# Kernel tuning notes

Measured on AMD Instinct MI355X. Metric: run time of the kernel, lower is better.

The kernel has to match this reference:

```python
import jax, jax.numpy as jnp
import numpy as np

SCALE_BASE = 512.0
GN_EPS = 1e-5


def _xpos(x, downscale):
    # x: [..., L, D]; XPOS rotary embedding with exponential length scale (torchscale)
    L, D = x.shape[-2], x.shape[-1]
    half = D // 2
    base = (jnp.arange(0, D, 2, dtype=jnp.float32) + 0.4 * D) / (1.4 * D)  # [half]
    min_pos = -(L // 2)
    power = (jnp.arange(min_pos, min_pos + L, dtype=jnp.float32) / SCALE_BASE)[:, None]
    scale = base[None, :] ** power  # [L, half]
    inv_freq = 1.0 / (10000.0 ** (jnp.arange(half, dtype=jnp.float32) / half))
    ang = jnp.arange(L, dtype=jnp.float32)[:, None] * inv_freq[None, :]  # [L, half]
    sin, cos = jnp.sin(ang), jnp.cos(ang)
    if downscale:
        scale = 1.0 / scale
    sin_s = jnp.repeat(sin * scale, 2, axis=-1)  # duplicate_interleave -> [L, D]
    cos_s = jnp.repeat(cos * scale, 2, axis=-1)
    x1, x2 = x[..., ::2], x[..., 1::2]
    rot = jnp.stack((-x2, x1), axis=-1).reshape(x.shape)  # rotate_every_two
    return x * cos_s + rot * sin_s


def _decay_mask(L, H):
    gammas = 1.0 - jnp.exp(jnp.linspace(np.log(1.0 / 32.0), np.log(1.0 / 512.0), H)).astype(jnp.float32)
    idx = jnp.arange(L)
    dist = idx[:, None] - idx[None, :]  # [L, L]
    causal = dist >= 0
    d = jnp.maximum(dist, 0).astype(jnp.float32)
    # gamma^|n-s| below diagonal, 0 above (gamma^inf = 0 in the torch version)
    return jnp.where(causal[None], gammas[:, None, None] ** d[None], 0.0)  # [H, L, L]


def setup_inputs() -> dict:
    key = jax.random.key(0)
    ks = jax.random.split(key, 9)
    B, L, D, H = 2, 2048, 1024, 16
    hd = D // H
    return {
        "query": jax.random.normal(ks[0], (B, L, D), jnp.float32),
        "key": jax.random.normal(ks[1], (B, L, D), jnp.float32),
        "value": jax.random.normal(ks[2], (B, L, D), jnp.float32),
        "W_Q": jax.random.normal(ks[3], (H, D, hd), jnp.float32) / D,
        "W_K": jax.random.normal(ks[4], (H, D, hd), jnp.float32) / D,
        "W_V": jax.random.normal(ks[5], (H, D, hd), jnp.float32) / D,
        "g_w": jax.random.normal(ks[6], (D, D), jnp.float32) * (2.0 / (D + D)) ** 0.5,
        "g_b": jnp.zeros((D,), jnp.float32),
        "out_w": jax.random.normal(ks[7], (D, D), jnp.float32) * (2.0 / (D + D)) ** 0.5,
        "out_b": jnp.zeros((D,), jnp.float32),
    }


def reference(query, key, value, W_Q, W_K, W_V, g_w, g_b, out_w, out_b):
    B, L, D = query.shape
    H = W_Q.shape[0]
    q = jnp.einsum('bld,hde->bhle', query, W_Q)
    k = jnp.einsum('bld,hde->bhle', key, W_K)
    v = jnp.einsum('bld,hde->bhle', value, W_V)
    q = _xpos(q, downscale=False)
    k = _xpos(k, downscale=True)
    # retention_parallel: QK^T * decay mask (no softmax, no scale), then @ V
    sim = jnp.einsum('bhnd,bhsd->bhns', q, k) * _decay_mask(L, H)[None]
    ret = jnp.einsum('bhns,bhsd->bhnd', sim, v)  # [B, H, L, hd]
    # GroupNorm(num_groups=H, affine=False) on (b n, h d): normalize per (b, h, n) over hd
    mu = ret.mean(axis=-1, keepdims=True)
    var = ret.var(axis=-1, keepdims=True)
    ret = (ret - mu) / jnp.sqrt(var + GN_EPS)
    ret = ret.transpose(0, 2, 1, 3).reshape(B, L, D)  # b h n d -> b n (h d)
    gate = jax.nn.silu(query @ g_w.T + g_b)
    return (ret * gate) @ out_w.T + out_b
```

## Files before the change

### kernel.cpp

```cpp
#include <hip/hip_runtime.h>
#include <cstdint>

#define B_  2
#define L_  2048
#define D_  1024
#define H_  16
#define HD_ 64
#define M_  (B_*L_)

#define MD  4194304u
#define DD  1048576u

#define OFF_XQB  0u
#define OFF_XKB  (MD)
#define OFF_XVB  (2u*MD)
#define OFF_WQT  (3u*MD)
#define OFF_WKT  (3u*MD + DD)
#define OFF_WVT  (3u*MD + 2u*DD)
#define OFF_GWB  (3u*MD + 3u*DD)
#define OFF_OWB  (3u*MD + 4u*DD)
#define OFF_GATE (3u*MD + 5u*DD)
#define OFF_QB2  (OFF_GATE + MD)
#define OFF_KB2  (OFF_QB2 + MD)
#define OFF_VTG  (OFF_KB2 + MD)
#define OFF_ABUF (OFF_VTG + MD)
#define OFF_F32  (OFF_ABUF + MD)

typedef __attribute__((ext_vector_type(8))) short bf16x8;
typedef __attribute__((ext_vector_type(4))) float f32x4;

__device__ __forceinline__ unsigned short f2b(float x){
  union { float f; unsigned u; } a; a.f = x;
  unsigned r = a.u + 0x7FFFu + ((a.u >> 16) & 1u);
  return (unsigned short)(r >> 16);
}
__device__ __forceinline__ float b2f(unsigned short u){
  union { unsigned u; float f; } a; a.u = ((unsigned)u) << 16; return a.f;
}

__global__ __launch_bounds__(256) void prep_kernel(
    const float* __restrict__ q, const float* __restrict__ k,
    const float* __restrict__ v, const float* __restrict__ gw,
    const float* __restrict__ ow, const float* __restrict__ WQ,
    const float* __restrict__ WK, const float* __restrict__ WV,
    unsigned short* __restrict__ ws)
{
  __shared__ float t[32][33];
  const int bx = blockIdx.x, tid = threadIdx.x;
  if (bx < 14336) {
    size_t i = ((size_t)bx * 256 + tid) * 4;
    const float* src; unsigned short* dst;
    if (i < MD)            { src = q  + i;              dst = ws + OFF_XQB + i; }
    else if (i < 2u*MD)    { src = k  + (i - MD);       dst = ws + OFF_XKB + (i - MD); }
    else if (i < 3u*MD)    { src = v  + (i - 2u*MD);    dst = ws + OFF_XVB + (i - 2u*MD); }
    else if (i < 3u*MD+DD) { src = gw + (i - 3u*MD);    dst = ws + OFF_GWB + (i - 3u*MD); }
    else                   { src = ow + (i - 3u*MD-DD); dst = ws + OFF_OWB + (i - 3u*MD - DD); }
    float4 vv = *(const float4*)src;
    ushort4 o; o.x = f2b(vv.x); o.y = f2b(vv.y); o.z = f2b(vv.z); o.w = f2b(vv.w);
    *(ushort4*)dst = o;
  } else if (bx < 17408) {
    const int tb = bx - 14336;
    const int w = tb >> 10;
    const int tb2 = tb & 1023;
    const int h = tb2 >> 6, tt = tb2 & 63;
    const int e0 = (tt & 1) * 32, d0 = (tt >> 1) * 32;
    const float* in = (w == 0) ? WQ : (w == 1) ? WK : WV;
    unsigned short* out = ws + ((w == 0) ? OFF_WQT : (w == 1) ? OFF_WKT : OFF_WVT);
    const int x = tid & 31, y0 = tid >> 5;
    for (int yy = y0; yy < 32; yy += 8)
      t[yy][x] = in[((size_t)h * D_ + d0 + yy) * HD_ + e0 + x];
    __syncthreads();
    for (int yy = y0; yy < 32; yy += 8)
      out[((size_t)h * HD_ + e0 + yy) * D_ + d0 + x] = f2b(t[x][yy]);
  } else {
    float* fb = (float*)(ws + OFF_F32);
    const int idx = (bx - 17408) * 256 + tid;
    const int l = idx >> 5, i = idx & 31;
    const float base = (2.0f * (float)i + 0.4f * (float)HD_) / (1.4f * (float)HD_);
    const float p = (float)(l - L_ / 2) * (1.0f / 512.0f);
    const float sc = exp2f(p * log2f(base));
    const float invf = exp2f(-(float)i * (13.287712379549449f / 32.0f));
    float s, c; sincosf((float)l * invf, &s, &c);
    fb[          l * 32 + i] = c * sc;
    fb[ 65536 +  l * 32 + i] = s * sc;
    const float is = 1.0f / sc;
    fb[131072 +  l * 32 + i] = c * is;
    fb[196608 +  l * 32 + i] = s * is;
  }
}

__device__ __forceinline__ void gemm_body(
    const unsigned short* __restrict__ A, const unsigned short* __restrict__ Bt,
    float* __restrict__ outF, unsigned short* __restrict__ outB,
    const float* __restrict__ ct, const float* __restrict__ st,
    const float* __restrict__ bias, int mode, int ldc, int M0, int N0,
    char* As, char* Bs)
{
  const int tid = threadIdx.x;
  const int wave = tid >> 6, lane = tid & 63;
  const int wm = wave & 1, wn = wave >> 1;
  const int mlane = lane & 15, kgrp = lane >> 4;
  const int srow = lane >> 2;
  const int scs  = lane & 3;
  const char* Ab = (const char*)A;
  const char* Bb = (const char*)Bt;

  f32x4 acc[4][4] = {};

  for (int K0 = 0; K0 < 1024; K0 += 32) {
    __syncthreads();
#pragma unroll
    for (int t = 0; t < 2; ++t) {
      const int row = wave * 32 + t * 16 + srow;
      const int gc = scs ^ ((row >> 1) & 3);
      const char* ga = Ab + ((size_t)(M0 + row) * 1024 + K0 + gc * 8) * 2;
      __builtin_amdgcn_global_load_lds(
          (const __attribute__((address_space(1))) void*)ga,
          (__attribute__((address_space(3))) void*)(As + (wave * 32 + t * 16) * 64 + lane * 16),
          16, 0, 0);
      const char* gb = Bb + ((size_t)(N0 + row) * 1024 + K0 + gc * 8) * 2;
      __builtin_amdgcn_global_load_lds(
          (const __attribute__((address_space(1))) void*)gb,
          (__attribute__((address_space(3))) void*)(Bs + (wave * 32 + t * 16) * 64 + lane * 16),
          16, 0, 0);
    }
    __syncthreads();
    bf16x8 af[4], bfr[4];
#pragma unroll
    for (int tm = 0; tm < 4; ++tm) {
      const int r = wm * 64 + tm * 16 + mlane;
      af[tm] = *(const bf16x8*)(As + r * 64 + ((kgrp ^ ((r >> 1) & 3)) << 4));
    }
#pragma unroll
    for (int tn = 0; tn < 4; ++tn) {
      const int r = wn * 64 + tn * 16 + mlane;
      bfr[tn] = *(const bf16x8*)(Bs + r * 64 + ((kgrp ^ ((r >> 1) & 3)) << 4));
    }
#pragma unroll
    for (int tm = 0; tm < 4; ++tm)
#pragma unroll
      for (int tn = 0; tn < 4; ++tn)
        acc[tm][tn] = __builtin_amdgcn_mfma_f32_16x16x32_bf16(af[tm], bfr[tn], acc[tm][tn], 0, 0, 0);
  }

#pragma unroll
  for (int tm = 0; tm < 4; ++tm)
#pragma unroll
    for (int tn = 0; tn < 4; ++tn) {
      f32x4 v = acc[tm][tn];
#pragma unroll
      for (int r = 0; r < 4; ++r) {
        const int grow = M0 + wm * 64 + tm * 16 + (lane >> 4) * 4 + r;
        const int gcol = N0 + wn * 64 + tn * 16 + mlane;
        float val = v[r];
        if (mode == 1 || mode == 2) {
          const float partner = __shfl_xor(val, 1);
          const int l = grow & (L_ - 1);
          const int i = (gcol >> 1) & 31;
          const float c = ct[l * 32 + i], s = st[l * 32 + i];
          val = (gcol & 1) ? (val * c + partner * s) : (val * c - partner * s);
          outB[(size_t)grow * ldc + gcol] = f2b(val);
        } else if (mode == 0) {
          outB[(size_t)grow * ldc + gcol] = f2b(val);
        } else if (mode == 3) {
          const float x = val + bias[gcol];
          outB[(size_t)grow * ldc + gcol] = f2b(x / (1.0f + expf(-x)));
        } else {
          outF[(size_t)grow * ldc + gcol] = val + bias[gcol];
        }
      }
    }
}

__global__ __launch_bounds__(256) void gemm4_kernel(
    unsigned short* __restrict__ ws, const float* __restrict__ g_b)
{
  __shared__ __align__(16) char As[128 * 64];
  __shared__ __align__(16) char Bs[128 * 64];
  const int z = blockIdx.y, bx = blockIdx.x;
  float* fb = (float*)(ws + OFF_F32);
  if (z == 0 && bx == 0 && threadIdx.x == 0)
    ((unsigned*)(fb + 262144))[0] = 0;
  const unsigned short *A, *Bt; unsigned short* outB;
  const float *ct = nullptr, *st = nullptr, *bias = nullptr;
  int mode, ldc, M0, N0;
  if (z == 0) {
    A = ws + OFF_XQB; Bt = ws + OFF_WQT; outB = ws + OFF_QB2;
    ct = fb; st = fb + 65536; mode = 1; ldc = D_;
    M0 = (bx & 31) * 128; N0 = (bx >> 5) * 128;
  } else if (z == 1) {
    A = ws + OFF_XKB; Bt = ws + OFF_WKT; outB = ws + OFF_KB2;
    ct = fb + 131072; st = fb + 196608; mode = 2; ldc = D_;
    M0 = (bx & 31) * 128; N0 = (bx >> 5) * 128;
  } else if (z == 2) {
    A = ws + OFF_WVT; Bt = ws + OFF_XVB; outB = ws + OFF_VTG;
    mode = 0; ldc = M_;
    M0 = (bx & 7) * 128; N0 = (bx >> 3) * 128;
  } else {
    A = ws + OFF_XQB; Bt = ws + OFF_GWB; outB = ws + OFF_GATE;
    bias = g_b; mode = 3; ldc = D_;
    M0 = (bx & 31) * 128; N0 = (bx >> 5) * 128;
  }
  gemm_body(A, Bt, nullptr, outB, ct, st, bias, mode, ldc, M0, N0, As, Bs);
}

__global__ __launch_bounds__(256) void gemm_final_kernel(
    unsigned short* __restrict__ ws, const float* __restrict__ out_b,
    float* __restrict__ out)
{
  __shared__ __align__(16) char As[128 * 64];
  __shared__ __align__(16) char Bs[128 * 64];
  gemm_body(ws + OFF_ABUF, ws + OFF_OWB, out, nullptr, nullptr, nullptr,
            out_b, 4, D_, blockIdx.x * 128, blockIdx.y * 128, As, Bs);
}

#define AQ_OFF 0
#define AK_OFF 8192
#define AV_OFF 16384
#define AP_OFF 24576

__global__ __launch_bounds__(256) void attn_mfma_kernel(
    const unsigned short* __restrict__ qg, const unsigned short* __restrict__ kg,
    const unsigned short* __restrict__ vtg, const unsigned short* __restrict__ gate,
    unsigned short* __restrict__ Abuf, unsigned* __restrict__ ctr)
{
  __shared__ __align__(16) char smem[32768];
  __shared__ unsigned s_item;
  const int tid = threadIdx.x, wave = tid >> 6, lane = tid & 63;
  const int mlane = lane & 15, kgrp = lane >> 4;
  const int rl = lane >> 3, csel = lane & 7;

  const float lo   = -3.4657359027997265f;
  const float step = -0.1848392481493187f;

  for (;;) {
    __syncthreads();
    if (tid == 0) s_item = atomicAdd(ctr, 1u);
    __syncthreads();
    const unsigned j = s_item;
    if (j >= 1024u) break;
    const int xq = 31 - (int)(j >> 5);
    const int bh = (int)(j & 31u), b = bh >> 4, h = bh & 15;
    const int l0 = xq * 64;

    const float gamma = 1.0f - expf(lo + (float)h * step);
    const float lg2g  = log2f(gamma);
    const float g1    = exp2f(-lg2g);
    const float gmr[4] = {1.0f, g1, g1 * g1, g1 * g1 * g1};

#pragma unroll
    for (int t = 0; t < 2; ++t) {
      const int row = 16 * wave + 8 * t + rl;
      const char* g = (const char*)(qg + (size_t)(b * L_ + l0 + row) * D_ + h * HD_ + ((csel ^ (row & 7)) << 3));
      __builtin_amdgcn_global_load_lds(
          (const __attribute__((address_space(1))) void*)g,
          (__attribute__((address_space(3))) void*)(smem + AQ_OFF + (16 * wave + 8 * t) * 128 + lane * 16),
          16, 0, 0);
    }
    __syncthreads();

    bf16x8 qa[2];
    {
      const int row = 16 * wave + mlane;
#pragma unroll
      for (int kk = 0; kk < 2; ++kk)
        qa[kk] = *(const bf16x8*)(smem + AQ_OFF + row * 128 + (((4 * kk + kgrp) ^ (row & 7)) << 4));
    }
    const float rqm = exp2f((float)(l0 + 16 * wave + mlane) * lg2g);

    f32x4 racc[4] = {};

    for (int it = 0; it <= xq; ++it) {
      const int s0 = it * 64;
      __syncthreads();
#pragma unroll
      for (int t = 0; t < 2; ++t) {
        const int row = 16 * wave + 8 * t + rl;
        const char* gk = (const char*)(kg + (size_t)(b * L_ + s0 + row) * D_ + h * HD_ + ((csel ^ (row & 7)) << 3));
        __builtin_amdgcn_global_load_lds(
            (const __attribute__((address_space(1))) void*)gk,
            (__attribute__((address_space(3))) void*)(smem + AK_OFF + (16 * wave + 8 * t) * 128 + lane * 16),
            16, 0, 0);
        const char* gv = (const char*)(vtg + (size_t)(h * HD_ + row) * M_ + b * L_ + s0 + ((csel ^ (row & 7)) << 3));
        __builtin_amdgcn_global_load_lds(
            (const __attribute__((address_space(1))) void*)gv,
            (__attribute__((address_space(3))) void*)(smem + AV_OFF + (16 * wave + 8 * t) * 128 + lane * 16),
            16, 0, 0);
      }
      __syncthreads();

      bf16x8 kb[4][2], vb[4][2];
#pragma unroll
      for (int tn = 0; tn < 4; ++tn)
#pragma unroll
        for (int kk = 0; kk < 2; ++kk) {
          const int row = 16 * tn + mlane;
          const int sw = ((4 * kk + kgrp) ^ (row & 7)) << 4;
          kb[tn][kk] = *(const bf16x8*)(smem + AK_OFF + row * 128 + sw);
          vb[tn][kk] = *(const bf16x8*)(smem + AV_OFF + row * 128 + sw);
        }
      float csb[4];
#pragma unroll
      for (int tn = 0; tn < 4; ++tn)
        csb[tn] = exp2f(-(float)(s0 + 16 * tn + 4 * kgrp) * lg2g);

      f32x4 sf[4];
#pragma unroll
      for (int tn = 0; tn < 4; ++tn) {
        f32x4 z = {};
        z = __builtin_amdgcn_mfma_f32_16x16x32_bf16(kb[tn][0], qa[0], z, 0, 0, 0);
        sf[tn] = __builtin_amdgcn_mfma_f32_16x16x32_bf16(kb[tn][1], qa[1], z, 0, 0, 0);
      }
      const int nrow = l0 + 16 * wave + mlane;
      const bool needMask = (it == xq);
      const int prow = 16 * wave + mlane;
#pragma unroll
      for (int tn = 0; tn < 4; ++tn) {
        const float wbase = rqm * csb[tn];
        const int sbase = s0 + 16 * tn + 4 * kgrp;
        float vv[4];
#pragma unroll
        for (int r = 0; r < 4; ++r) {
          float w = wbase * gmr[r];
          if (needMask) w = (nrow - (sbase + r) >= 0) ? w : 0.0f;
          vv[r] = sf[tn][r] * w;
        }
        uint2 pk;
        pk.x = (unsigned)f2b(vv[0]) | ((unsigned)f2b(vv[1]) << 16);
        pk.y = (unsigned)f2b(vv[2]) | ((unsigned)f2b(vv[3]) << 16);
        *(uint2*)(smem + AP_OFF + prow * 128 +
                  (((2 * tn + (kgrp >> 1)) ^ (prow & 7)) << 4) + ((kgrp & 1) << 3)) = pk;
      }
      bf16x8 pa[2];
#pragma unroll
      for (int kk = 0; kk < 2; ++kk) {
        const int row = 16 * wave + mlane;
        pa[kk] = *(const bf16x8*)(smem + AP_OFF + row * 128 + (((4 * kk + kgrp) ^ (row & 7)) << 4));
      }
#pragma unroll
      for (int tn = 0; tn < 4; ++tn) {
        racc[tn] = __builtin_amdgcn_mfma_f32_16x16x32_bf16(pa[0], vb[tn][0], racc[tn], 0, 0, 0);
        racc[tn] = __builtin_amdgcn_mfma_f32_16x16x32_bf16(pa[1], vb[tn][1], racc[tn], 0, 0, 0);
      }
    }

#pragma unroll
    for (int r = 0; r < 4; ++r) {
      float vv[4], sm = 0.0f, sq = 0.0f;
#pragma unroll
      for (int tn = 0; tn < 4; ++tn) {
        vv[tn] = racc[tn][r];
        sm += vv[tn]; sq += vv[tn] * vv[tn];
      }
#pragma unroll
      for (int off = 1; off < 16; off <<= 1) {
        sm += __shfl_xor(sm, off);
        sq += __shfl_xor(sq, off);
      }
      const float mu = sm * (1.0f / 64.0f);
      float var = sq * (1.0f / 64.0f) - mu * mu;
      var = fmaxf(var, 0.0f);
      const float inv = rsqrtf(var + 1e-5f);
      const int row = l0 + 16 * wave + kgrp * 4 + r;
      const size_t base = (size_t)(b * L_ + row) * D_ + h * HD_;
#pragma unroll
      for (int tn = 0; tn < 4; ++tn) {
        const int c = 16 * tn + mlane;
        const float g = b2f(gate[base + c]);
        Abuf[base + c] = f2b((vv[tn] - mu) * inv * g);
      }
    }
  }
}

extern "C" void kernel_launch(void* const* d_in, const int* in_sizes, int n_in,
                              void* d_out, int out_size, void* d_ws, size_t ws_size,
                              hipStream_t stream)
{
  const float* query = (const float*)d_in[0];
  const float* key   = (const float*)d_in[1];
  const float* value = (const float*)d_in[2];
  const float* W_Q   = (const float*)d_in[3];
  const float* W_K   = (const float*)d_in[4];
  const float* W_V   = (const float*)d_in[5];
  const float* g_b   = (const float*)d_in[7];
  const float* out_b = (const float*)d_in[9];
  float* out = (float*)d_out;

  unsigned short* ws = (unsigned short*)d_ws;
  float* fb = (float*)(ws + OFF_F32);
  unsigned* ctr = (unsigned*)(fb + 262144);

  prep_kernel<<<17664, 256, 0, stream>>>(query, key, value,
                                         (const float*)d_in[6],
                                         (const float*)d_in[8],
                                         W_Q, W_K, W_V, ws);

  gemm4_kernel<<<dim3(256, 4), 256, 0, stream>>>(ws, g_b);

  attn_mfma_kernel<<<512, 256, 0, stream>>>(ws + OFF_QB2, ws + OFF_KB2,
                                            ws + OFF_VTG, ws + OFF_GATE,
                                            ws + OFF_ABUF, ctr);

  gemm_final_kernel<<<dim3(32, 8), 256, 0, stream>>>(ws, out_b, out);
}
```

Before: 268.7 us.

## Retile GEMMs to 128x64 with K=64 steps and statically pair attention work

The shared GEMM body moves from 128x128 tiles with 32-wide K steps to 128x64 tiles with 64-wide K steps and an 8-way XOR swizzle. The GEMM grids double, so there are more blocks to fill the compute units, and there are half as many K-loop barriers. The attention kernel drops its atomic work-queue counter. Each block now handles a fixed pair of query tiles (p and 31-p) to balance the causal workload, and a __syncthreads is added before P is read back from LDS. In exchange, each block reuses less A data and issues an extra barrier per attention iteration.

```diff
diff --git a/kernel.cpp b/kernel.cpp
--- a/kernel.cpp
+++ b/kernel.cpp
@@ -27,6 +27,7 @@
 #define OFF_F32  (OFF_ABUF + MD)
 
 typedef __attribute__((ext_vector_type(8))) short bf16x8;
+typedef __attribute__((ext_vector_type(4))) short s16x4;
 typedef __attribute__((ext_vector_type(4))) float f32x4;
 
 __device__ __forceinline__ unsigned short f2b(float x){
@@ -100,58 +101,65 @@
   const int wave = tid >> 6, lane = tid & 63;
   const int wm = wave & 1, wn = wave >> 1;
   const int mlane = lane & 15, kgrp = lane >> 4;
-  const int srow = lane >> 2;
-  const int scs  = lane & 3;
+  const int rl = lane >> 3, csel = lane & 7;
   const char* Ab = (const char*)A;
   const char* Bb = (const char*)Bt;
 
-  f32x4 acc[4][4] = {};
-
-  for (int K0 = 0; K0 < 1024; K0 += 32) {
+  f32x4 acc[4][2] = {};
+
+  for (int K0 = 0; K0 < 1024; K0 += 64) {
     __syncthreads();
 #pragma unroll
-    for (int t = 0; t < 2; ++t) {
-      const int row = wave * 32 + t * 16 + srow;
-      const int gc = scs ^ ((row >> 1) & 3);
-      const char* ga = Ab + ((size_t)(M0 + row) * 1024 + K0 + gc * 8) * 2;
+    for (int t = 0; t < 4; ++t) {
+      const int row = wave * 32 + t * 8 + rl;
+      const int gc = csel ^ (row & 7);
+      const char* ga = Ab + ((size_t)(M0 + row) * 1024 + K0) * 2 + gc * 16;
       __builtin_amdgcn_global_load_lds(
           (const __attribute__((address_space(1))) void*)ga,
-          (__attribute__((address_space(3))) void*)(As + (wave * 32 + t * 16) * 64 + lane * 16),
+          (__attribute__((address_space(3))) void*)(As + (wave * 32 + t * 8) * 128 + lane * 16),
           16, 0, 0);
-      const char* gb = Bb + ((size_t)(N0 + row) * 1024 + K0 + gc * 8) * 2;
+    }
+#pragma unroll
+    for (int t = 0; t < 2; ++t) {
+      const int row = wave * 16 + t * 8 + rl;
+      const int gc = csel ^ (row & 7);
+      const char* gb = Bb + ((size_t)(N0 + row) * 1024 + K0) * 2 + gc * 16;
       __builtin_amdgcn_global_load_lds(
           (const __attribute__((address_space(1))) void*)gb,
-          (__attribute__((address_space(3))) void*)(Bs + (wave * 32 + t * 16) * 64 + lane * 16),
+          (__attribute__((address_space(3))) void*)(Bs + (wave * 16 + t * 8) * 128 + lane * 16),
           16, 0, 0);
     }
     __syncthreads();
-    bf16x8 af[4], bfr[4];
-#pragma unroll
-    for (int tm = 0; tm < 4; ++tm) {
-      const int r = wm * 64 + tm * 16 + mlane;
-      af[tm] = *(const bf16x8*)(As + r * 64 + ((kgrp ^ ((r >> 1) & 3)) << 4));
-    }
-#pragma unroll
-    for (int tn = 0; tn < 4; ++tn) {
-      const int r = wn * 64 + tn * 16 + mlane;
-      bfr[tn] = *(const bf16x8*)(Bs + r * 64 + ((kgrp ^ ((r >> 1) & 3)) << 4));
-    }
-#pragma unroll
-    for (int tm = 0; tm < 4; ++tm)
-#pragma unroll
-      for (int tn = 0; tn < 4; ++tn)
-        acc[tm][tn] = __builtin_amdgcn_mfma_f32_16x16x32_bf16(af[tm], bfr[tn], acc[tm][tn], 0, 0, 0);
+#pragma unroll
+    for (int kh = 0; kh < 2; ++kh) {
+      bf16x8 af[4], bfr[2];
+#pragma unroll
+      for (int tm = 0; tm < 4; ++tm) {
+        const int r = wm * 64 + tm * 16 + mlane;
+        af[tm] = *(const bf16x8*)(As + r * 128 + (((kh * 4 + kgrp) ^ (r & 7)) << 4));
+      }
+#pragma unroll
+      for (int tn = 0; tn < 2; ++tn) {
+        const int r = wn * 32 + tn * 16 + mlane;
+        bfr[tn] = *(const bf16x8*)(Bs + r * 128 + (((kh * 4 + kgrp) ^ (r & 7)) << 4));
+      }
+#pragma unroll
+      for (int tm = 0; tm < 4; ++tm)
+#pragma unroll
+        for (int tn = 0; tn < 2; ++tn)
+          acc[tm][tn] = __builtin_amdgcn_mfma_f32_16x16x32_bf16(af[tm], bfr[tn], acc[tm][tn], 0, 0, 0);
+    }
   }
 
 #pragma unroll
   for (int tm = 0; tm < 4; ++tm)
 #pragma unroll
-    for (int tn = 0; tn < 4; ++tn) {
+    for (int tn = 0; tn < 2; ++tn) {
       f32x4 v = acc[tm][tn];
 #pragma unroll
       for (int r = 0; r < 4; ++r) {
         const int grow = M0 + wm * 64 + tm * 16 + (lane >> 4) * 4 + r;
-        const int gcol = N0 + wn * 64 + tn * 16 + mlane;
+        const int gcol = N0 + wn * 32 + tn * 16 + mlane;
         float val = v[r];
         if (mode == 1 || mode == 2) {
           const float partner = __shfl_xor(val, 1);
@@ -175,31 +183,29 @@
 __global__ __launch_bounds__(256) void gemm4_kernel(
     unsigned short* __restrict__ ws, const float* __restrict__ g_b)
 {
-  __shared__ __align__(16) char As[128 * 64];
-  __shared__ __align__(16) char Bs[128 * 64];
+  __shared__ __align__(16) char As[128 * 128];
+  __shared__ __align__(16) char Bs[64 * 128];
   const int z = blockIdx.y, bx = blockIdx.x;
   float* fb = (float*)(ws + OFF_F32);
-  if (z == 0 && bx == 0 && threadIdx.x == 0)
-    ((unsigned*)(fb + 262144))[0] = 0;
   const unsigned short *A, *Bt; unsigned short* outB;
   const float *ct = nullptr, *st = nullptr, *bias = nullptr;
   int mode, ldc, M0, N0;
   if (z == 0) {
     A = ws + OFF_XQB; Bt = ws + OFF_WQT; outB = ws + OFF_QB2;
     ct = fb; st = fb + 65536; mode = 1; ldc = D_;
-    M0 = (bx & 31) * 128; N0 = (bx >> 5) * 128;
+    M0 = (bx & 31) * 128; N0 = (bx >> 5) * 64;
   } else if (z == 1) {
     A = ws + OFF_XKB; Bt = ws + OFF_WKT; outB = ws + OFF_KB2;
     ct = fb + 131072; st = fb + 196608; mode = 2; ldc = D_;
-    M0 = (bx & 31) * 128; N0 = (bx >> 5) * 128;
+    M0 = (bx & 31) * 128; N0 = (bx >> 5) * 64;
   } else if (z == 2) {
     A = ws + OFF_WVT; Bt = ws + OFF_XVB; outB = ws + OFF_VTG;
     mode = 0; ldc = M_;
-    M0 = (bx & 7) * 128; N0 = (bx >> 3) * 128;
+    M0 = (bx & 7) * 128; N0 = (bx >> 3) * 64;
   } else {
     A = ws + OFF_XQB; Bt = ws + OFF_GWB; outB = ws + OFF_GATE;
     bias = g_b; mode = 3; ldc = D_;
-    M0 = (bx & 31) * 128; N0 = (bx >> 5) * 128;
+    M0 = (bx & 31) * 128; N0 = (bx >> 5) * 64;
   }
   gemm_body(A, Bt, nullptr, outB, ct, st, bias, mode, ldc, M0, N0, As, Bs);
 }
@@ -208,10 +214,10 @@
     unsigned short* __restrict__ ws, const float* __restrict__ out_b,
     float* __restrict__ out)
 {
-  __shared__ __align__(16) char As[128 * 64];
-  __shared__ __align__(16) char Bs[128 * 64];
+  __shared__ __align__(16) char As[128 * 128];
+  __shared__ __align__(16) char Bs[64 * 128];
   gemm_body(ws + OFF_ABUF, ws + OFF_OWB, out, nullptr, nullptr, nullptr,
-            out_b, 4, D_, blockIdx.x * 128, blockIdx.y * 128, As, Bs);
+            out_b, 4, D_, blockIdx.x * 128, blockIdx.y * 64, As, Bs);
 }
 
 #define AQ_OFF 0
@@ -222,32 +228,30 @@
 __global__ __launch_bounds__(256) void attn_mfma_kernel(
     const unsigned short* __restrict__ qg, const unsigned short* __restrict__ kg,
     const unsigned short* __restrict__ vtg, const unsigned short* __restrict__ gate,
-    unsigned short* __restrict__ Abuf, unsigned* __restrict__ ctr)
+    unsigned short* __restrict__ Abuf)
 {
   __shared__ __align__(16) char smem[32768];
-  __shared__ unsigned s_item;
   const int tid = threadIdx.x, wave = tid >> 6, lane = tid & 63;
   const int mlane = lane & 15, kgrp = lane >> 4;
   const int rl = lane >> 3, csel = lane & 7;
 
+  const int id = blockIdx.x;
+  const int bh = id & 31, p = id >> 5;
+  const int b = bh >> 4, h = bh & 15;
+
   const float lo   = -3.4657359027997265f;
   const float step = -0.1848392481493187f;
-
-  for (;;) {
+  const float gamma = 1.0f - expf(lo + (float)h * step);
+  const float lg2g  = log2f(gamma);
+  const float g1    = exp2f(-lg2g);
+  const float gmr[4] = {1.0f, g1, g1 * g1, g1 * g1 * g1};
+
+#pragma unroll 1
+  for (int half = 0; half < 2; ++half) {
+    const int xq = half ? (31 - p) : p;
+    const int l0 = xq * 64;
+
     __syncthreads();
-    if (tid == 0) s_item = atomicAdd(ctr, 1u);
-    __syncthreads();
-    const unsigned j = s_item;
-    if (j >= 1024u) break;
-    const int xq = 31 - (int)(j >> 5);
-    const int bh = (int)(j & 31u), b = bh >> 4, h = bh & 15;
-    const int l0 = xq * 64;
-
-    const float gamma = 1.0f - expf(lo + (float)h * step);
-    const float lg2g  = log2f(gamma);
-    const float g1    = exp2f(-lg2g);
-    const float gmr[4] = {1.0f, g1, g1 * g1, g1 * g1 * g1};
-
 #pragma unroll
     for (int t = 0; t < 2; ++t) {
       const int row = 16 * wave + 8 * t + rl;
@@ -325,12 +329,13 @@
           if (needMask) w = (nrow - (sbase + r) >= 0) ? w : 0.0f;
           vv[r] = sf[tn][r] * w;
         }
-        uint2 pk;
-        pk.x = (unsigned)f2b(vv[0]) | ((unsigned)f2b(vv[1]) << 16);
-        pk.y = (unsigned)f2b(vv[2]) | ((unsigned)f2b(vv[3]) << 16);
-        *(uint2*)(smem + AP_OFF + prow * 128 +
+        s16x4 pk;
+        pk[0] = (short)f2b(vv[0]); pk[1] = (short)f2b(vv[1]);
+        pk[2] = (short)f2b(vv[2]); pk[3] = (short)f2b(vv[3]);
+        *(s16x4*)(smem + AP_OFF + prow * 128 +
                   (((2 * tn + (kgrp >> 1)) ^ (prow & 7)) << 4) + ((kgrp & 1) << 3)) = pk;
       }
+      __syncthreads();
       bf16x8 pa[2];
 #pragma unroll
       for (int kk = 0; kk < 2; ++kk) {
@@ -388,19 +393,17 @@
   float* out = (float*)d_out;
 
   unsigned short* ws = (unsigned short*)d_ws;
-  float* fb = (float*)(ws + OFF_F32);
-  unsigned* ctr = (unsigned*)(fb + 262144);
 
   prep_kernel<<<17664, 256, 0, stream>>>(query, key, value,
                                          (const float*)d_in[6],
                                          (const float*)d_in[8],
                                          W_Q, W_K, W_V, ws);
 
-  gemm4_kernel<<<dim3(256, 4), 256, 0, stream>>>(ws, g_b);
+  gemm4_kernel<<<dim3(512, 4), 256, 0, stream>>>(ws, g_b);
 
   attn_mfma_kernel<<<512, 256, 0, stream>>>(ws + OFF_QB2, ws + OFF_KB2,
                                             ws + OFF_VTG, ws + OFF_GATE,
-                                            ws + OFF_ABUF, ctr);
-
-  gemm_final_kernel<<<dim3(32, 8), 256, 0, stream>>>(ws, out_b, out);
-}
+                                            ws + OFF_ABUF);
+
+  gemm_final_kernel<<<dim3(32, 16), 256, 0, stream>>>(ws, out_b, out);
+}
```

Result: faster. 236.0 us (-12.2%).
